# Kernel tuning notes

Hardware: AMD Instinct MI355X
Metric: run time of the kernel (lower is better)

## Reference

```python
import jax, jax.numpy as jnp
import numpy as np

N = 100000
E = 3200000
F_IN = 128
HID = 64
NUM_GRAPHS = 512
NUM_CLASSES = 2


def setup_inputs() -> dict:
    key = jax.random.key(0)
    ks = jax.random.split(key, 8)
    x = jax.random.normal(ks[0], (N, F_IN), dtype=jnp.float32)
    edge_index = jax.random.randint(ks[1], (2, E), 0, N, dtype=jnp.int64)
    batch = jnp.sort(jax.random.randint(ks[2], (N,), 0, NUM_GRAPHS, dtype=jnp.int64))
    # Glorot-style init for GCN weights, PyTorch default-style for fc
    W1 = jax.random.normal(ks[3], (F_IN, HID), dtype=jnp.float32) * (1.0 / np.sqrt(F_IN))
    b1 = jnp.zeros((HID,), dtype=jnp.float32)
    W2 = jax.random.normal(ks[4], (HID, HID), dtype=jnp.float32) * (1.0 / np.sqrt(HID))
    b2 = jnp.zeros((HID,), dtype=jnp.float32)
    Wfc = jax.random.normal(ks[5], (HID, NUM_CLASSES), dtype=jnp.float32) * (1.0 / np.sqrt(HID))
    bfc = jax.random.normal(ks[6], (NUM_CLASSES,), dtype=jnp.float32) * 0.01
    return {"x": x, "edge_index": edge_index, "batch": batch,
            "W1": W1, "b1": b1, "W2": W2, "b2": b2, "Wfc": Wfc, "bfc": bfc}


def _gcn_conv(x, row, col, deg_inv_sqrt, W, b):
    """PyG GCNConv: out[col] += d^{-1/2}[row] d^{-1/2}[col] * (x W)[row], self-loops included in row/col."""
    h = x @ W  # [N, out_dim]
    norm = deg_inv_sqrt[row] * deg_inv_sqrt[col]  # [E+N]
    msgs = h[row] * norm[:, None]  # gather + scale
    out = jax.ops.segment_sum(msgs, col, num_segments=N)  # scatter-add
    return out + b


def reference(x, edge_index, batch, W1, b1, W2, b2, Wfc, bfc):
    # add self-loops once (shared normalization for both layers)
    loop = jnp.arange(N, dtype=edge_index.dtype)
    row = jnp.concatenate([edge_index[0], loop])  # sources
    col = jnp.concatenate([edge_index[1], loop])  # targets
    deg = jax.ops.segment_sum(jnp.ones_like(col, dtype=x.dtype), col, num_segments=N)
    deg_inv_sqrt = jnp.where(deg > 0, jax.lax.rsqrt(deg), 0.0)

    h = jax.nn.relu(_gcn_conv(x, row, col, deg_inv_sqrt, W1, b1))
    h = jax.nn.relu(_gcn_conv(h, row, col, deg_inv_sqrt, W2, b2))

    # global_mean_pool over batch ids
    sums = jax.ops.segment_sum(h, batch, num_segments=NUM_GRAPHS)  # [G, HID]
    counts = jax.ops.segment_sum(jnp.ones((N,), dtype=h.dtype), batch, num_segments=NUM_GRAPHS)
    pooled = sums / jnp.maximum(counts, 1.0)[:, None]

    # dropout p=0.5 is identity in eval mode
    return pooled @ Wfc + bfc  # [G, NUM_CLASSES]
```

## Files before the change

kernel.cpp:

```cpp
#include <hip/hip_runtime.h>

#define N_NODES   100000
#define N_EDGES   3200000
#define F_INP     128
#define HID       64
#define N_GRAPHS  512
#define N_CLASSES 2
#define NB        782
#define SCAT_BLOCKS 256
#define CHUNK     (N_EDGES / SCAT_BLOCKS)

__device__ __forceinline__ unsigned short f2bf(float f) {
    unsigned int u = __float_as_uint(f);
    return (unsigned short)((u + 0x7FFFu + ((u >> 16) & 1u)) >> 16);
}
__device__ __forceinline__ float bf_lo(unsigned int u) { return __uint_as_float(u << 16); }
__device__ __forceinline__ float bf_hi(unsigned int u) { return __uint_as_float(u & 0xFFFF0000u); }

__global__ __launch_bounds__(256) void hist_kernel(const int* __restrict__ ei,
                                                   int* __restrict__ bcnt,
                                                   int* __restrict__ bh) {
    __shared__ int hist[NB];
    for (int i = threadIdx.x; i < NB; i += 256) hist[i] = 0;
    __syncthreads();
    const int e0 = blockIdx.x * CHUNK, e1 = e0 + CHUNK;
    for (int e = e0 + threadIdx.x; e < e1; e += 256)
        atomicAdd(&hist[ei[N_EDGES + e] >> 7], 1);
    __syncthreads();
    for (int i = threadIdx.x; i < NB; i += 256) {
        int v = hist[i];
        bh[(size_t)blockIdx.x * NB + i] = v;
        if (v) atomicAdd(&bcnt[i], v);
    }
}

__global__ __launch_bounds__(1024) void scan_kernel(const int* __restrict__ bcnt,
                                                    int* __restrict__ boff) {
    __shared__ int s[1024];
    const int tid = threadIdx.x;
    const int v = (tid < NB) ? bcnt[tid] : 0;
    s[tid] = v;
    __syncthreads();
    for (int d = 1; d < 1024; d <<= 1) {
        int t = (tid >= d) ? s[tid - d] : 0;
        __syncthreads();
        s[tid] += t;
        __syncthreads();
    }
    if (tid <= NB) boff[tid] = s[tid] - v;
}

__global__ __launch_bounds__(64) void bbase_kernel(int* __restrict__ bh,
                                                   const int* __restrict__ boff) {
    const int b = blockIdx.x * 64 + threadIdx.x;
    if (b >= NB) return;
    int base = boff[b];
    for (int i = 0; i < SCAT_BLOCKS; i += 8) {
        int v[8];
#pragma unroll
        for (int j = 0; j < 8; ++j) v[j] = bh[(size_t)(i + j) * NB + b];
#pragma unroll
        for (int j = 0; j < 8; ++j) { bh[(size_t)(i + j) * NB + b] = base; base += v[j]; }
    }
}

__global__ __launch_bounds__(256) void scatter_kernel(const int* __restrict__ ei,
                                                      const int* __restrict__ bh,
                                                      int* __restrict__ pairs) {
    __shared__ int lbase[NB];
    __shared__ int lcur[NB];
    for (int i = threadIdx.x; i < NB; i += 256) {
        lbase[i] = bh[(size_t)blockIdx.x * NB + i];
        lcur[i] = 0;
    }
    __syncthreads();
    const int e0 = blockIdx.x * CHUNK, e1 = e0 + CHUNK;
    for (int e = e0 + threadIdx.x; e < e1; e += 256) {
        int c = ei[N_EDGES + e];
        int r = ei[e];
        int b = c >> 7;
        int off = atomicAdd(&lcur[b], 1);
        pairs[lbase[b] + off] = r | ((c & 127) << 17);
    }
}

__global__ __launch_bounds__(256) void csr_kernel(const int* __restrict__ pairs,
                                                  const int* __restrict__ boff,
                                                  int* __restrict__ adj,
                                                  int* __restrict__ offs,
                                                  float* __restrict__ dis) {
    __shared__ int cnt[128];
    __shared__ int sc[128];
    __shared__ int base[128];
    __shared__ int cur[128];
    const int tid = threadIdx.x;
    const int b = blockIdx.x;
    const int beg = boff[b], end = boff[b + 1];
    if (tid < 128) { cnt[tid] = 0; cur[tid] = 0; }
    __syncthreads();
    for (int e = beg + tid; e < end; e += 256)
        atomicAdd(&cnt[pairs[e] >> 17], 1);
    __syncthreads();
    if (tid < 128) sc[tid] = cnt[tid];
    __syncthreads();
    for (int d = 1; d < 128; d <<= 1) {
        int t = (tid >= d && tid < 128) ? sc[tid - d] : 0;
        __syncthreads();
        if (tid < 128) sc[tid] += t;
        __syncthreads();
    }
    if (tid < 128) base[tid] = beg + sc[tid] - cnt[tid];
    __syncthreads();
    for (int e = beg + tid; e < end; e += 256) {
        int v = pairs[e];
        int lc = v >> 17;
        int o = atomicAdd(&cur[lc], 1);
        adj[base[lc] + o] = v & 131071;
    }
    const int n = (b << 7) + tid;
    if (tid < 128 && n < N_NODES) {
        offs[n] = base[tid];
        dis[n] = rsqrtf((float)cnt[tid] + 1.0f);
    }
    if (b == 0 && tid == 0) offs[N_NODES] = N_EDGES;
}

__global__ __launch_bounds__(256) void mm1_kernel(const float* __restrict__ x,
                                                  const float* __restrict__ W1,
                                                  const float* __restrict__ dis,
                                                  unsigned short* __restrict__ p) {
    __shared__ float xs[64 * F_INP];
    __shared__ float ws[F_INP * HID];
    for (int i = threadIdx.x; i < F_INP * HID / 4; i += 256)
        ((float4*)ws)[i] = ((const float4*)W1)[i];
    const long base4 = (long)blockIdx.x * (64 * F_INP / 4);
    const long tot4 = (long)N_NODES * F_INP / 4;
    for (int i = threadIdx.x; i < 64 * F_INP / 4; i += 256) {
        float4 v = make_float4(0.f, 0.f, 0.f, 0.f);
        if (base4 + i < tot4) v = ((const float4*)x)[base4 + i];
        ((float4*)xs)[i] = v;
    }
    __syncthreads();
    const int tx = threadIdx.x & 15;
    const int ty = threadIdx.x >> 4;
    const int row0 = blockIdx.x * 64 + ty * 4;
    float acc[4][4] = {};
#pragma unroll 4
    for (int k = 0; k < F_INP; k += 4) {
        float4 a[4];
#pragma unroll
        for (int i = 0; i < 4; ++i)
            a[i] = *(const float4*)(xs + (ty * 4 + i) * F_INP + k);
        float4 w0 = *(const float4*)(ws + (k + 0) * HID + tx * 4);
        float4 w1 = *(const float4*)(ws + (k + 1) * HID + tx * 4);
        float4 w2 = *(const float4*)(ws + (k + 2) * HID + tx * 4);
        float4 w3 = *(const float4*)(ws + (k + 3) * HID + tx * 4);
#pragma unroll
        for (int i = 0; i < 4; ++i) {
            acc[i][0] += a[i].x * w0.x + a[i].y * w1.x + a[i].z * w2.x + a[i].w * w3.x;
            acc[i][1] += a[i].x * w0.y + a[i].y * w1.y + a[i].z * w2.y + a[i].w * w3.y;
            acc[i][2] += a[i].x * w0.z + a[i].y * w1.z + a[i].z * w2.z + a[i].w * w3.z;
            acc[i][3] += a[i].x * w0.w + a[i].y * w1.w + a[i].z * w2.w + a[i].w * w3.w;
        }
    }
#pragma unroll
    for (int i = 0; i < 4; ++i) {
        int rr = row0 + i;
        if (rr < N_NODES) {
            float d = dis[rr];
            ushort4 o;
            o.x = f2bf(d * acc[i][0]);
            o.y = f2bf(d * acc[i][1]);
            o.z = f2bf(d * acc[i][2]);
            o.w = f2bf(d * acc[i][3]);
            *(ushort4*)(p + (size_t)rr * HID + tx * 4) = o;
        }
    }
}

__global__ __launch_bounds__(256) void mm2_kernel(const unsigned short* __restrict__ hb,
                                                  const float* __restrict__ W2,
                                                  const float* __restrict__ dis,
                                                  unsigned short* __restrict__ p) {
    __shared__ unsigned short hs[64 * HID];
    __shared__ float ws[HID * HID];
    for (int i = threadIdx.x; i < HID * HID / 4; i += 256)
        ((float4*)ws)[i] = ((const float4*)W2)[i];
    const long base8 = (long)blockIdx.x * (64 * HID / 8);
    const long tot8 = (long)N_NODES * HID / 8;
    for (int i = threadIdx.x; i < 64 * HID / 8; i += 256) {
        uint4 v = make_uint4(0u, 0u, 0u, 0u);
        if (base8 + i < tot8) v = ((const uint4*)hb)[base8 + i];
        ((uint4*)hs)[i] = v;
    }
    __syncthreads();
    const int tx = threadIdx.x & 15;
    const int ty = threadIdx.x >> 4;
    const int row0 = blockIdx.x * 64 + ty * 4;
    float acc[4][4] = {};
#pragma unroll 2
    for (int k = 0; k < HID; k += 8) {
        uint4 a[4];
#pragma unroll
        for (int i = 0; i < 4; ++i)
            a[i] = *(const uint4*)(hs + (ty * 4 + i) * HID + k);
        float4 w[8];
#pragma unroll
        for (int m = 0; m < 8; ++m)
            w[m] = *(const float4*)(ws + (k + m) * HID + tx * 4);
#pragma unroll
        for (int i = 0; i < 4; ++i) {
            float h0 = bf_lo(a[i].x), h1 = bf_hi(a[i].x);
            float h2 = bf_lo(a[i].y), h3 = bf_hi(a[i].y);
            float h4 = bf_lo(a[i].z), h5 = bf_hi(a[i].z);
            float h6 = bf_lo(a[i].w), h7 = bf_hi(a[i].w);
            acc[i][0] += h0 * w[0].x + h1 * w[1].x + h2 * w[2].x + h3 * w[3].x
                       + h4 * w[4].x + h5 * w[5].x + h6 * w[6].x + h7 * w[7].x;
            acc[i][1] += h0 * w[0].y + h1 * w[1].y + h2 * w[2].y + h3 * w[3].y
                       + h4 * w[4].y + h5 * w[5].y + h6 * w[6].y + h7 * w[7].y;
            acc[i][2] += h0 * w[0].z + h1 * w[1].z + h2 * w[2].z + h3 * w[3].z
                       + h4 * w[4].z + h5 * w[5].z + h6 * w[6].z + h7 * w[7].z;
            acc[i][3] += h0 * w[0].w + h1 * w[1].w + h2 * w[2].w + h3 * w[3].w
                       + h4 * w[4].w + h5 * w[5].w + h6 * w[6].w + h7 * w[7].w;
        }
    }
#pragma unroll
    for (int i = 0; i < 4; ++i) {
        int rr = row0 + i;
        if (rr < N_NODES) {
            float d = dis[rr];
            ushort4 o;
            o.x = f2bf(d * acc[i][0]);
            o.y = f2bf(d * acc[i][1]);
            o.z = f2bf(d * acc[i][2]);
            o.w = f2bf(d * acc[i][3]);
            *(ushort4*)(p + (size_t)rr * HID + tx * 4) = o;
        }
    }
}

__device__ __forceinline__ float gather_node(const unsigned short* __restrict__ p,
                                             const int* __restrict__ adj,
                                             int c, int beg, int end, int q, int g) {
    float acc[8];
    {
        uint4 s = *(const uint4*)(p + (size_t)c * HID + g * 8);
        float sm = (q == 0) ? 1.f : 0.f;
        acc[0] = sm * bf_lo(s.x); acc[1] = sm * bf_hi(s.x);
        acc[2] = sm * bf_lo(s.y); acc[3] = sm * bf_hi(s.y);
        acc[4] = sm * bf_lo(s.z); acc[5] = sm * bf_hi(s.z);
        acc[6] = sm * bf_lo(s.w); acc[7] = sm * bf_hi(s.w);
    }
    int e = beg;
    for (; e + 32 <= end; e += 32) {
        int r0 = adj[e + q];
        int r1 = adj[e + 8 + q];
        int r2 = adj[e + 16 + q];
        int r3 = adj[e + 24 + q];
        uint4 v0 = *(const uint4*)(p + (size_t)r0 * HID + g * 8);
        uint4 v1 = *(const uint4*)(p + (size_t)r1 * HID + g * 8);
        uint4 v2 = *(const uint4*)(p + (size_t)r2 * HID + g * 8);
        uint4 v3 = *(const uint4*)(p + (size_t)r3 * HID + g * 8);
        acc[0] += (bf_lo(v0.x) + bf_lo(v1.x)) + (bf_lo(v2.x) + bf_lo(v3.x));
        acc[1] += (bf_hi(v0.x) + bf_hi(v1.x)) + (bf_hi(v2.x) + bf_hi(v3.x));
        acc[2] += (bf_lo(v0.y) + bf_lo(v1.y)) + (bf_lo(v2.y) + bf_lo(v3.y));
        acc[3] += (bf_hi(v0.y) + bf_hi(v1.y)) + (bf_hi(v2.y) + bf_hi(v3.y));
        acc[4] += (bf_lo(v0.z) + bf_lo(v1.z)) + (bf_lo(v2.z) + bf_lo(v3.z));
        acc[5] += (bf_hi(v0.z) + bf_hi(v1.z)) + (bf_hi(v2.z) + bf_hi(v3.z));
        acc[6] += (bf_lo(v0.w) + bf_lo(v1.w)) + (bf_lo(v2.w) + bf_lo(v3.w));
        acc[7] += (bf_hi(v0.w) + bf_hi(v1.w)) + (bf_hi(v2.w) + bf_hi(v3.w));
    }
    for (; e + 16 <= end; e += 16) {
        int r0 = adj[e + q];
        int r1 = adj[e + 8 + q];
        uint4 v0 = *(const uint4*)(p + (size_t)r0 * HID + g * 8);
        uint4 v1 = *(const uint4*)(p + (size_t)r1 * HID + g * 8);
        acc[0] += bf_lo(v0.x) + bf_lo(v1.x); acc[1] += bf_hi(v0.x) + bf_hi(v1.x);
        acc[2] += bf_lo(v0.y) + bf_lo(v1.y); acc[3] += bf_hi(v0.y) + bf_hi(v1.y);
        acc[4] += bf_lo(v0.z) + bf_lo(v1.z); acc[5] += bf_hi(v0.z) + bf_hi(v1.z);
        acc[6] += bf_lo(v0.w) + bf_lo(v1.w); acc[7] += bf_hi(v0.w) + bf_hi(v1.w);
    }
    for (; e < end; e += 8) {
        int idx = e + q;
        int r = adj[min(idx, end - 1)];
        float m = (idx < end) ? 1.f : 0.f;
        uint4 v = *(const uint4*)(p + (size_t)r * HID + g * 8);
        acc[0] = fmaf(m, bf_lo(v.x), acc[0]); acc[1] = fmaf(m, bf_hi(v.x), acc[1]);
        acc[2] = fmaf(m, bf_lo(v.y), acc[2]); acc[3] = fmaf(m, bf_hi(v.y), acc[3]);
        acc[4] = fmaf(m, bf_lo(v.z), acc[4]); acc[5] = fmaf(m, bf_hi(v.z), acc[5]);
        acc[6] = fmaf(m, bf_lo(v.w), acc[6]); acc[7] = fmaf(m, bf_hi(v.w), acc[7]);
    }
    const bool q0 = (q & 1) != 0, q1 = (q & 2) != 0, q2 = (q & 4) != 0;
    float b0 = (q0 ? acc[1] : acc[0]) + __shfl_xor(q0 ? acc[0] : acc[1], 8, 64);
    float b1 = (q0 ? acc[3] : acc[2]) + __shfl_xor(q0 ? acc[2] : acc[3], 8, 64);
    float b2 = (q0 ? acc[5] : acc[4]) + __shfl_xor(q0 ? acc[4] : acc[5], 8, 64);
    float b3 = (q0 ? acc[7] : acc[6]) + __shfl_xor(q0 ? acc[6] : acc[7], 8, 64);
    float c0 = (q1 ? b1 : b0) + __shfl_xor(q1 ? b0 : b1, 16, 64);
    float c1 = (q1 ? b3 : b2) + __shfl_xor(q1 ? b2 : b3, 16, 64);
    return (q2 ? c1 : c0) + __shfl_xor(q2 ? c0 : c1, 32, 64);
}

__global__ __launch_bounds__(256) void gather1_kernel(const unsigned short* __restrict__ p,
                                                      const int* __restrict__ adj,
                                                      const int* __restrict__ offs,
                                                      const float* __restrict__ dis,
                                                      const float* __restrict__ b1,
                                                      unsigned short* __restrict__ hb) {
    const int lane = threadIdx.x & 63;
    const int q = lane >> 3, g = lane & 7;
    const int gwave = (blockIdx.x * blockDim.x + threadIdx.x) >> 6;
    const int nwaves = (gridDim.x * blockDim.x) >> 6;
    const int per = (N_NODES + nwaves - 1) / nwaves;
    const int c0 = gwave * per;
    const int c1 = min(N_NODES, c0 + per);
    const float bj = b1[g * 8 + q];
    for (int c = c0; c < c1; ++c) {
        const int beg = offs[c], end = offs[c + 1];
        float val = gather_node(p, adj, c, beg, end, q, g);
        hb[(size_t)c * HID + g * 8 + q] = f2bf(fmaxf(dis[c] * val + bj, 0.f));
    }
}

__global__ __launch_bounds__(256) void gather2_kernel(const unsigned short* __restrict__ p,
                                                      const int* __restrict__ adj,
                                                      const int* __restrict__ offs,
                                                      const float* __restrict__ dis,
                                                      const float* __restrict__ b2,
                                                      const int* __restrict__ batch,
                                                      float* __restrict__ sums) {
    const int lane = threadIdx.x & 63;
    const int q = lane >> 3, g = lane & 7;
    const int gwave = (blockIdx.x * blockDim.x + threadIdx.x) >> 6;
    const int nwaves = (gridDim.x * blockDim.x) >> 6;
    const int per = (N_NODES + nwaves - 1) / nwaves;
    const int c0 = gwave * per;
    const int c1 = min(N_NODES, c0 + per);
    const float bj = b2[g * 8 + q];
    const int feat = g * 8 + q;
    float part = 0.f;
    int gc = -1;
    for (int c = c0; c < c1; ++c) {
        const int beg = offs[c], end = offs[c + 1];
        float val = gather_node(p, adj, c, beg, end, q, g);
        float v = fmaxf(dis[c] * val + bj, 0.f);
        int gid = batch[c];
        if (gid != gc) {
            if (gc >= 0) atomicAdd(&sums[(size_t)gc * HID + feat], part);
            part = 0.f;
            gc = gid;
        }
        part += v;
    }
    if (gc >= 0) atomicAdd(&sums[(size_t)gc * HID + feat], part);
}

__global__ void fc_kernel(const float* __restrict__ sums, const int* __restrict__ batch,
                          const float* __restrict__ Wfc, const float* __restrict__ bfc,
                          float* __restrict__ out) {
    const int g = blockIdx.x;
    const int j = threadIdx.x;
    int lo = 0, hi = N_NODES;
    while (lo < hi) { int m = (lo + hi) >> 1; if (batch[m] < g) lo = m + 1; else hi = m; }
    const int l0 = lo;
    lo = 0; hi = N_NODES;
    while (lo < hi) { int m = (lo + hi) >> 1; if (batch[m] < g + 1) lo = m + 1; else hi = m; }
    float cnt = fmaxf((float)(lo - l0), 1.0f);
    float pj = sums[(size_t)g * HID + j] / cnt;
    float a0 = pj * Wfc[j * N_CLASSES + 0];
    float a1 = pj * Wfc[j * N_CLASSES + 1];
    for (int off = 32; off > 0; off >>= 1) {
        a0 += __shfl_down(a0, off, 64);
        a1 += __shfl_down(a1, off, 64);
    }
    if (j == 0) {
        out[g * N_CLASSES + 0] = a0 + bfc[0];
        out[g * N_CLASSES + 1] = a1 + bfc[1];
    }
}

extern "C" void kernel_launch(void* const* d_in, const int* in_sizes, int n_in,
                              void* d_out, int out_size, void* d_ws, size_t ws_size,
                              hipStream_t stream) {
    const float* x     = (const float*)d_in[0];
    const int*   ei    = (const int*)d_in[1];
    const int*   batch = (const int*)d_in[2];
    const float* W1    = (const float*)d_in[3];
    const float* b1    = (const float*)d_in[4];
    const float* W2    = (const float*)d_in[5];
    const float* b2    = (const float*)d_in[6];
    const float* Wfc   = (const float*)d_in[7];
    const float* bfc   = (const float*)d_in[8];
    float* out = (float*)d_out;

    char* ws = (char*)d_ws;
    size_t off = 0;
    auto alloc = [&](size_t bytes) -> void* {
        void* pp = ws + off;
        off += (bytes + 255) & ~(size_t)255;
        return pp;
    };
    int*   bcnt   = (int*)alloc((size_t)NB * 4);
    int*   boff   = (int*)alloc((size_t)(NB + 1) * 4);
    int*   bh     = (int*)alloc((size_t)SCAT_BLOCKS * NB * 4);
    float* dis    = (float*)alloc((size_t)N_NODES * 4);
    int*   pairs  = (int*)alloc((size_t)N_EDGES * 4);
    int*   adj    = (int*)alloc((size_t)N_EDGES * 4);
    int*   offs   = (int*)alloc((size_t)(N_NODES + 1) * 4);
    unsigned short* p  = (unsigned short*)alloc((size_t)N_NODES * HID * 2);
    unsigned short* hb = (unsigned short*)alloc((size_t)N_NODES * HID * 2);
    float* sums   = (float*)alloc((size_t)N_GRAPHS * HID * 4);

    hipMemsetAsync(bcnt, 0, (size_t)NB * 4, stream);
    hipMemsetAsync(sums, 0, (size_t)N_GRAPHS * HID * 4, stream);

    hist_kernel<<<SCAT_BLOCKS, 256, 0, stream>>>(ei, bcnt, bh);
    scan_kernel<<<1, 1024, 0, stream>>>(bcnt, boff);
    bbase_kernel<<<(NB + 63) / 64, 64, 0, stream>>>(bh, boff);
    scatter_kernel<<<SCAT_BLOCKS, 256, 0, stream>>>(ei, bh, pairs);
    csr_kernel<<<NB, 256, 0, stream>>>(pairs, boff, adj, offs, dis);
    mm1_kernel<<<(N_NODES + 63) / 64, 256, 0, stream>>>(x, W1, dis, p);
    gather1_kernel<<<2048, 256, 0, stream>>>(p, adj, offs, dis, b1, hb);
    mm2_kernel<<<(N_NODES + 63) / 64, 256, 0, stream>>>(hb, W2, dis, p);
    gather2_kernel<<<2048, 256, 0, stream>>>(p, adj, offs, dis, b2, batch, sums);
    fc_kernel<<<N_GRAPHS, 64, 0, stream>>>(sums, batch, Wfc, bfc, out);
}
```

Before: 360.3 us.

## Pad shared tiles, shrink mm1 row tile, balance gather waves by edge count

The mm1 tile shrinks from 64 to 32 rows, which gives smaller shared memory use and higher occupancy. Both matmul kernels now pad their shared-memory row stride and map threads to rows strided by 16 instead of contiguous rows, to avoid LDS bank conflicts. The gather kernels assign each wave a node range found by binary search over CSR offsets, so each wave gets an equal share of edges instead of an equal number of nodes. The search adds a small per-wave setup cost. With random uniform degrees the node-based split was probably already fairly balanced.

```diff
diff --git a/kernel.cpp b/kernel.cpp
--- a/kernel.cpp
+++ b/kernel.cpp
@@ -125,47 +125,48 @@
     if (b == 0 && tid == 0) offs[N_NODES] = N_EDGES;
 }
 
+#define MM1_ROWS 32
+#define XS_LD    132
 __global__ __launch_bounds__(256) void mm1_kernel(const float* __restrict__ x,
                                                   const float* __restrict__ W1,
                                                   const float* __restrict__ dis,
                                                   unsigned short* __restrict__ p) {
-    __shared__ float xs[64 * F_INP];
+    __shared__ float xs[MM1_ROWS * XS_LD];
     __shared__ float ws[F_INP * HID];
     for (int i = threadIdx.x; i < F_INP * HID / 4; i += 256)
         ((float4*)ws)[i] = ((const float4*)W1)[i];
-    const long base4 = (long)blockIdx.x * (64 * F_INP / 4);
-    const long tot4 = (long)N_NODES * F_INP / 4;
-    for (int i = threadIdx.x; i < 64 * F_INP / 4; i += 256) {
+    const int row_base = blockIdx.x * MM1_ROWS;
+    for (int i = threadIdx.x; i < MM1_ROWS * (F_INP / 4); i += 256) {
+        int r = i >> 5, c4 = i & 31;
+        int gr = row_base + r;
         float4 v = make_float4(0.f, 0.f, 0.f, 0.f);
-        if (base4 + i < tot4) v = ((const float4*)x)[base4 + i];
-        ((float4*)xs)[i] = v;
+        if (gr < N_NODES) v = *(const float4*)(x + (size_t)gr * F_INP + c4 * 4);
+        *(float4*)(xs + r * XS_LD + c4 * 4) = v;
     }
     __syncthreads();
     const int tx = threadIdx.x & 15;
     const int ty = threadIdx.x >> 4;
-    const int row0 = blockIdx.x * 64 + ty * 4;
-    float acc[4][4] = {};
+    float acc[2][4] = {};
 #pragma unroll 4
     for (int k = 0; k < F_INP; k += 4) {
-        float4 a[4];
-#pragma unroll
-        for (int i = 0; i < 4; ++i)
-            a[i] = *(const float4*)(xs + (ty * 4 + i) * F_INP + k);
+        float4 a0 = *(const float4*)(xs + ty * XS_LD + k);
+        float4 a1 = *(const float4*)(xs + (ty + 16) * XS_LD + k);
         float4 w0 = *(const float4*)(ws + (k + 0) * HID + tx * 4);
         float4 w1 = *(const float4*)(ws + (k + 1) * HID + tx * 4);
         float4 w2 = *(const float4*)(ws + (k + 2) * HID + tx * 4);
         float4 w3 = *(const float4*)(ws + (k + 3) * HID + tx * 4);
-#pragma unroll
-        for (int i = 0; i < 4; ++i) {
-            acc[i][0] += a[i].x * w0.x + a[i].y * w1.x + a[i].z * w2.x + a[i].w * w3.x;
-            acc[i][1] += a[i].x * w0.y + a[i].y * w1.y + a[i].z * w2.y + a[i].w * w3.y;
-            acc[i][2] += a[i].x * w0.z + a[i].y * w1.z + a[i].z * w2.z + a[i].w * w3.z;
-            acc[i][3] += a[i].x * w0.w + a[i].y * w1.w + a[i].z * w2.w + a[i].w * w3.w;
-        }
-    }
-#pragma unroll
-    for (int i = 0; i < 4; ++i) {
-        int rr = row0 + i;
+        acc[0][0] += a0.x * w0.x + a0.y * w1.x + a0.z * w2.x + a0.w * w3.x;
+        acc[0][1] += a0.x * w0.y + a0.y * w1.y + a0.z * w2.y + a0.w * w3.y;
+        acc[0][2] += a0.x * w0.z + a0.y * w1.z + a0.z * w2.z + a0.w * w3.z;
+        acc[0][3] += a0.x * w0.w + a0.y * w1.w + a0.z * w2.w + a0.w * w3.w;
+        acc[1][0] += a1.x * w0.x + a1.y * w1.x + a1.z * w2.x + a1.w * w3.x;
+        acc[1][1] += a1.x * w0.y + a1.y * w1.y + a1.z * w2.y + a1.w * w3.y;
+        acc[1][2] += a1.x * w0.z + a1.y * w1.z + a1.z * w2.z + a1.w * w3.z;
+        acc[1][3] += a1.x * w0.w + a1.y * w1.w + a1.z * w2.w + a1.w * w3.w;
+    }
+#pragma unroll
+    for (int i = 0; i < 2; ++i) {
+        int rr = row_base + ty + 16 * i;
         if (rr < N_NODES) {
             float d = dis[rr];
             ushort4 o;
@@ -178,32 +179,33 @@
     }
 }
 
+#define HS_LD 72
 __global__ __launch_bounds__(256) void mm2_kernel(const unsigned short* __restrict__ hb,
                                                   const float* __restrict__ W2,
                                                   const float* __restrict__ dis,
                                                   unsigned short* __restrict__ p) {
-    __shared__ unsigned short hs[64 * HID];
+    __shared__ unsigned short hs[64 * HS_LD];
     __shared__ float ws[HID * HID];
     for (int i = threadIdx.x; i < HID * HID / 4; i += 256)
         ((float4*)ws)[i] = ((const float4*)W2)[i];
-    const long base8 = (long)blockIdx.x * (64 * HID / 8);
-    const long tot8 = (long)N_NODES * HID / 8;
-    for (int i = threadIdx.x; i < 64 * HID / 8; i += 256) {
+    const int row_base = blockIdx.x * 64;
+    for (int i = threadIdx.x; i < 64 * (HID / 8); i += 256) {
+        int r = i >> 3, c8 = i & 7;
+        int gr = row_base + r;
         uint4 v = make_uint4(0u, 0u, 0u, 0u);
-        if (base8 + i < tot8) v = ((const uint4*)hb)[base8 + i];
-        ((uint4*)hs)[i] = v;
+        if (gr < N_NODES) v = *(const uint4*)(hb + (size_t)gr * HID + c8 * 8);
+        *(uint4*)(hs + r * HS_LD + c8 * 8) = v;
     }
     __syncthreads();
     const int tx = threadIdx.x & 15;
     const int ty = threadIdx.x >> 4;
-    const int row0 = blockIdx.x * 64 + ty * 4;
     float acc[4][4] = {};
 #pragma unroll 2
     for (int k = 0; k < HID; k += 8) {
         uint4 a[4];
 #pragma unroll
         for (int i = 0; i < 4; ++i)
-            a[i] = *(const uint4*)(hs + (ty * 4 + i) * HID + k);
+            a[i] = *(const uint4*)(hs + (ty + 16 * i) * HS_LD + k);
         float4 w[8];
 #pragma unroll
         for (int m = 0; m < 8; ++m)
@@ -226,7 +228,7 @@
     }
 #pragma unroll
     for (int i = 0; i < 4; ++i) {
-        int rr = row0 + i;
+        int rr = row_base + ty + 16 * i;
         if (rr < N_NODES) {
             float d = dis[rr];
             ushort4 o;
@@ -237,6 +239,19 @@
             *(ushort4*)(p + (size_t)rr * HID + tx * 4) = o;
         }
     }
+}
+
+__device__ __forceinline__ void wave_range(const int* __restrict__ offs, int w, int nwaves,
+                                           int& c0, int& c1) {
+    const int per = (N_EDGES + nwaves - 1) / nwaves;
+    const int s0 = w * per;
+    const int s1 = s0 + per;
+    int lo = 0, hi = N_NODES;
+    while (lo < hi) { int m = (lo + hi) >> 1; if (offs[m] < s0) lo = m + 1; else hi = m; }
+    c0 = lo;
+    hi = N_NODES;
+    while (lo < hi) { int m = (lo + hi) >> 1; if (offs[m] < s1) lo = m + 1; else hi = m; }
+    c1 = lo;
 }
 
 __device__ __forceinline__ float gather_node(const unsigned short* __restrict__ p,
@@ -310,9 +325,8 @@
     const int q = lane >> 3, g = lane & 7;
     const int gwave = (blockIdx.x * blockDim.x + threadIdx.x) >> 6;
     const int nwaves = (gridDim.x * blockDim.x) >> 6;
-    const int per = (N_NODES + nwaves - 1) / nwaves;
-    const int c0 = gwave * per;
-    const int c1 = min(N_NODES, c0 + per);
+    int c0, c1;
+    wave_range(offs, gwave, nwaves, c0, c1);
     const float bj = b1[g * 8 + q];
     for (int c = c0; c < c1; ++c) {
         const int beg = offs[c], end = offs[c + 1];
@@ -332,9 +346,8 @@
     const int q = lane >> 3, g = lane & 7;
     const int gwave = (blockIdx.x * blockDim.x + threadIdx.x) >> 6;
     const int nwaves = (gridDim.x * blockDim.x) >> 6;
-    const int per = (N_NODES + nwaves - 1) / nwaves;
-    const int c0 = gwave * per;
-    const int c1 = min(N_NODES, c0 + per);
+    int c0, c1;
+    wave_range(offs, gwave, nwaves, c0, c1);
     const float bj = b2[g * 8 + q];
     const int feat = g * 8 + q;
     float part = 0.f;
@@ -418,7 +431,7 @@
     bbase_kernel<<<(NB + 63) / 64, 64, 0, stream>>>(bh, boff);
     scatter_kernel<<<SCAT_BLOCKS, 256, 0, stream>>>(ei, bh, pairs);
     csr_kernel<<<NB, 256, 0, stream>>>(pairs, boff, adj, offs, dis);
-    mm1_kernel<<<(N_NODES + 63) / 64, 256, 0, stream>>>(x, W1, dis, p);
+    mm1_kernel<<<(N_NODES + MM1_ROWS - 1) / MM1_ROWS, 256, 0, stream>>>(x, W1, dis, p);
     gather1_kernel<<<2048, 256, 0, stream>>>(p, adj, offs, dis, b1, hb);
     mm2_kernel<<<(N_NODES + 63) / 64, 256, 0, stream>>>(hb, W2, dis, p);
     gather2_kernel<<<2048, 256, 0, stream>>>(p, adj, offs, dis, b2, batch, sums);
```

After: 370.0 us. 2.7% more time.
